# Optimization experiments

Hardware: AMD Instinct MI355X
Metric: run time of the kernel (lower is better)

## Reference

```python
import jax, jax.numpy as jnp
import numpy as np

B, L, D, H = 2, 2048, 1024, 16
HD = D // H  # head_dim = 64


def setup_inputs() -> dict:
    key = jax.random.key(0)
    k1, k2, k3 = jax.random.split(key, 3)
    x = jax.random.normal(k1, (B, L, D), dtype=jnp.float32)
    # nn.Linear(d_model, 3*d_model): weight [3D, D], bias [3D]
    lim = 1.0 / np.sqrt(D)
    W_qkv = jax.random.uniform(k2, (3 * D, D), dtype=jnp.float32, minval=-lim, maxval=lim)
    b_qkv = jax.random.uniform(k3, (3 * D,), dtype=jnp.float32, minval=-lim, maxval=lim)
    return {"x": x, "W_qkv": W_qkv, "b_qkv": b_qkv}


def reference(x, W_qkv, b_qkv):
    b, l, d = x.shape
    qkv = x @ W_qkv.T + b_qkv                      # [b, l, 3d]
    q, k, v = jnp.split(qkv, 3, axis=-1)           # each [b, l, d]
    # split heads: [b, l, h, hd]
    q = q.reshape(b, l, H, HD)
    k = k.reshape(b, l, H, HD)
    v = v.reshape(b, l, H, HD)
    scale = 1.0 / np.sqrt(HD).astype(np.float32)
    # scores [b, h, l, l]
    scores = jnp.einsum('bqhd,bkhd->bhqk', q, k) * scale
    attn = jax.nn.softmax(scores, axis=-1)
    out = jnp.einsum('bhqk,bkhd->bqhd', attn, v)   # [b, l, h, hd]
    return out.reshape(b, l, d)
```

## Files before the change

### kernel.cpp

```cpp
#include <hip/hip_runtime.h>

#define BATCH 2
#define SEQ 2048
#define DMODEL 1024
#define NH 16
#define HD 64
#define M_TOT (BATCH*SEQ)
#define N_TOT (3*DMODEL)
#define K_TOT (DMODEL)

typedef __attribute__((ext_vector_type(8)))  _Float16 f16x8;
typedef __attribute__((ext_vector_type(4)))  float    f32x4;
typedef __attribute__((ext_vector_type(16))) float    f32x16;

static __device__ __forceinline__ unsigned short f2h(float f) {
  _Float16 h = (_Float16)f;
  return __builtin_bit_cast(unsigned short, h);
}

static __device__ __forceinline__ f32x16 zero16() {
  f32x16 z;
  #pragma unroll
  for (int i = 0; i < 16; ++i) z[i] = 0.f;
  return z;
}

static __device__ __forceinline__ void async16(const unsigned short* g, unsigned short* l) {
  __builtin_amdgcn_global_load_lds(
      (const __attribute__((address_space(1))) unsigned*)g,
      (__attribute__((address_space(3))) unsigned*)l, 16, 0, 0);
}

__global__ __launch_bounds__(256) void cast_f16(
    const float* __restrict__ src, unsigned short* __restrict__ dst, int n8)
{
  int i = blockIdx.x * 256 + threadIdx.x;
  if (i >= n8) return;
  float4 v0 = ((const float4*)src)[2*i];
  float4 v1 = ((const float4*)src)[2*i + 1];
  uint4 pk;
  pk.x = (unsigned)f2h(v0.x) | ((unsigned)f2h(v0.y) << 16);
  pk.y = (unsigned)f2h(v0.z) | ((unsigned)f2h(v0.w) << 16);
  pk.z = (unsigned)f2h(v1.x) | ((unsigned)f2h(v1.y) << 16);
  pk.w = (unsigned)f2h(v1.z) | ((unsigned)f2h(v1.w) << 16);
  ((uint4*)dst)[i] = pk;
}

__global__ __launch_bounds__(256) void qkv_gemm_mfma(
    const unsigned short* __restrict__ A,
    const unsigned short* __restrict__ B,
    const float* __restrict__ bias,
    unsigned short* __restrict__ C)
{
  __shared__ unsigned short As[128][32];
  __shared__ unsigned short Bs[128][32];

  const int tid  = threadIdx.x;
  const int wave = tid >> 6;
  const int lane = tid & 63;
  const int l15  = lane & 15;
  const int quad = lane >> 4;

  const int n0 = blockIdx.x * 128;
  const int m0 = blockIdx.y * 128;
  const int wm = (wave & 1) * 64;
  const int wn = (wave >> 1) * 64;

  f32x4 acc[4][4];
  #pragma unroll
  for (int i = 0; i < 4; ++i)
    #pragma unroll
    for (int j = 0; j < 4; ++j) acc[i][j] = (f32x4){0.f,0.f,0.f,0.f};

  const int srow = tid >> 2;
  const int skc  = (tid & 3) * 8;
  const unsigned short* Ag0 = A + (size_t)(m0 + srow) * K_TOT + skc;
  const unsigned short* Ag1 = A + (size_t)(m0 + 64 + srow) * K_TOT + skc;
  const unsigned short* Bg0 = B + (size_t)(n0 + srow) * K_TOT + skc;
  const unsigned short* Bg1 = B + (size_t)(n0 + 64 + srow) * K_TOT + skc;
  unsigned short* Al0 = &As[0][0] + tid * 8;
  unsigned short* Al1 = Al0 + 2048;
  unsigned short* Bl0 = &Bs[0][0] + tid * 8;
  unsigned short* Bl1 = Bl0 + 2048;

  for (int k0 = 0; k0 < K_TOT; k0 += 32) {
    __syncthreads();
    async16(Ag0 + k0, Al0);
    async16(Ag1 + k0, Al1);
    async16(Bg0 + k0, Bl0);
    async16(Bg1 + k0, Bl1);
    __syncthreads();

    f16x8 af[4], bf[4];
    #pragma unroll
    for (int i = 0; i < 4; ++i)
      af[i] = *(const f16x8*)&As[wm + i*16 + l15][quad*8];
    #pragma unroll
    for (int j = 0; j < 4; ++j)
      bf[j] = *(const f16x8*)&Bs[wn + j*16 + l15][quad*8];

    #pragma unroll
    for (int i = 0; i < 4; ++i)
      #pragma unroll
      for (int j = 0; j < 4; ++j)
        acc[i][j] = __builtin_amdgcn_mfma_f32_16x16x32_f16(af[i], bf[j], acc[i][j], 0, 0, 0);
  }

  float bv[4];
  #pragma unroll
  for (int j = 0; j < 4; ++j) bv[j] = bias[n0 + wn + j*16 + l15];

  #pragma unroll
  for (int i = 0; i < 4; ++i) {
    #pragma unroll
    for (int j = 0; j < 4; ++j) {
      #pragma unroll
      for (int r = 0; r < 4; ++r) {
        const size_t row = (size_t)(m0 + wm + i*16 + quad*4 + r);
        C[row * N_TOT + n0 + wn + j*16 + l15] = f2h(acc[i][j][r] + bv[j]);
      }
    }
  }
}

__global__ __launch_bounds__(256) void attn_mfma2(
    const unsigned short* __restrict__ qkv, float* __restrict__ out)
{
  __shared__ unsigned short Ks[64][72];
  __shared__ unsigned short Vt[64][72];
  __shared__ unsigned short Ps[4][32][72];
  __shared__ float Dn[4][32];

  const int tid  = threadIdx.x;
  const int wv   = tid >> 6;
  const int lane = tid & 63;
  const int l31  = lane & 31;
  const int h32  = lane >> 5;
  const int qsw  = l31 >> 3;

  const int qt = blockIdx.x;
  const int hh = blockIdx.y;
  const int b  = blockIdx.z;
  const int q0 = qt*128 + wv*32;

  f16x8 qf[4];
  {
    const unsigned short* qrow = qkv + (size_t)(b*SEQ + q0 + l31) * N_TOT + hh*HD;
    #pragma unroll
    for (int f = 0; f < 4; ++f)
      qf[f] = *(const f16x8*)(qrow + f*16 + h32*8);
  }

  f32x16 oacc[2];
  oacc[0] = zero16();
  oacc[1] = zero16();
  float dsum = 0.f;

  const unsigned short* kg = qkv + (size_t)b*SEQ*N_TOT + DMODEL   + hh*HD;
  const unsigned short* vg = qkv + (size_t)b*SEQ*N_TOT + 2*DMODEL + hh*HD;

  for (int kt = 0; kt < SEQ/64; ++kt) {
    const int k0 = kt * 64;
    __syncthreads();

    #pragma unroll
    for (int i = 0; i < 2; ++i) {
      int f   = tid + 256*i;
      int key = f >> 3, c = f & 7;
      const unsigned short* src = kg + (size_t)(k0 + key) * N_TOT + c*8;
      int sc = c ^ ((key >> 3) & 7);
      *(uint4*)&Ks[key][sc*8] = *(const uint4*)src;
    }
    {
      int key = tid >> 2;
      int d0  = (tid & 3) * 16;
      const unsigned short* src = vg + (size_t)(k0 + key) * N_TOT + d0;
      union { uint4 v; unsigned short s[8]; } u0, u1;
      u0.v = *(const uint4*)src;
      u1.v = *(const uint4*)(src + 8);
      const int kgrp = key >> 3, klow = key & 7;
      #pragma unroll
      for (int j = 0; j < 8; ++j) {
        int dd = d0 + j;
        Vt[dd][((kgrp ^ ((dd >> 3) & 7)) * 8) + klow] = u0.s[j];
        dd = d0 + 8 + j;
        Vt[dd][((kgrp ^ ((dd >> 3) & 7)) * 8) + klow] = u1.s[j];
      }
    }
    __syncthreads();

    f32x16 sa[2];
    sa[0] = zero16();
    sa[1] = zero16();
    #pragma unroll
    for (int f = 0; f < 4; ++f) {
      const int g = f*2 + h32;
      #pragma unroll
      for (int kb = 0; kb < 2; ++kb) {
        const int row = kb*32 + l31;
        f16x8 kf = *(const f16x8*)&Ks[row][((g ^ ((row >> 3) & 7)) * 8)];
        sa[kb] = __builtin_amdgcn_mfma_f32_32x32x16_f16(kf, qf[f], sa[kb], 0, 0, 0);
      }
    }

    #pragma unroll
    for (int kb = 0; kb < 2; ++kb) {
      #pragma unroll
      for (int g4 = 0; g4 < 4; ++g4) {
        unsigned short hsv[4];
        #pragma unroll
        for (int r = 0; r < 4; ++r) {
          float p = __expf(0.125f * sa[kb][g4*4 + r]);
          dsum += p;
          hsv[r] = f2h(p);
        }
        unsigned short* dst =
            &Ps[wv][l31][(((kb*4 + g4) ^ qsw) & 7) * 8 + h32*4];
        uint2 pk;
        pk.x = (unsigned)hsv[0] | ((unsigned)hsv[1] << 16);
        pk.y = (unsigned)hsv[2] | ((unsigned)hsv[3] << 16);
        *(uint2*)dst = pk;
      }
    }

    #pragma unroll
    for (int f = 0; f < 4; ++f) {
      const int g = f*2 + h32;
      f16x8 pf = *(const f16x8*)&Ps[wv][l31][((g ^ qsw) & 7) * 8];
      #pragma unroll
      for (int jd = 0; jd < 2; ++jd) {
        const int row = jd*32 + l31;
        f16x8 vf = *(const f16x8*)&Vt[row][((g ^ ((row >> 3) & 7)) * 8)];
        oacc[jd] = __builtin_amdgcn_mfma_f32_32x32x16_f16(pf, vf, oacc[jd], 0, 0, 0);
      }
    }
  }

  dsum += __shfl_xor(dsum, 32, 64);
  Dn[wv][l31] = 1.f / dsum;

  #pragma unroll
  for (int jd = 0; jd < 2; ++jd) {
    #pragma unroll
    for (int g4 = 0; g4 < 4; ++g4) {
      #pragma unroll
      for (int r = 0; r < 4; ++r) {
        const int qrow = g4*8 + h32*4 + r;
        const float oval = oacc[jd][g4*4 + r] * Dn[wv][qrow];
        out[(size_t)(b*SEQ + q0 + qrow) * DMODEL + hh*HD + jd*32 + l31] = oval;
      }
    }
  }
}

extern "C" void kernel_launch(void* const* d_in, const int* in_sizes, int n_in,
                              void* d_out, int out_size, void* d_ws, size_t ws_size,
                              hipStream_t stream) {
  const float* x    = (const float*)d_in[0];
  const float* W    = (const float*)d_in[1];
  const float* bias = (const float*)d_in[2];
  float* out = (float*)d_out;

  unsigned short* qkv = (unsigned short*)d_ws;
  unsigned short* xh  = qkv + (size_t)M_TOT * N_TOT;
  unsigned short* Wh  = xh  + (size_t)M_TOT * K_TOT;

  cast_f16<<<(M_TOT*K_TOT/8 + 255)/256, 256, 0, stream>>>(x, xh, M_TOT*K_TOT/8);
  cast_f16<<<(N_TOT*K_TOT/8 + 255)/256, 256, 0, stream>>>(W, Wh, N_TOT*K_TOT/8);

  dim3 g1(N_TOT/128, M_TOT/128);
  qkv_gemm_mfma<<<g1, 256, 0, stream>>>(xh, Wh, bias, qkv);

  dim3 g2(SEQ/128, NH, BATCH);
  attn_mfma2<<<g2, 256, 0, stream>>>(qkv, out);
}
```

Baseline: 191.4 us.

## Emit transposed V from GEMM, double-buffer async K/V loads in attention

The QKV GEMM now writes Q and K into a packed buffer, with Q pre-scaled by log2(e)/sqrt(hd), and computes V^T directly by swapping operands so V lands per head in transposed layout. The GEMM K-step grows to 64 with a rotated LDS swizzle. The attention kernel uses global_load_lds to double-buffer K and V tiles, with manual waitcnt and barriers. It also switches to exp2f and raises wave priority around the MFMA blocks. This removes the per-tile scalar transposition of V in LDS and overlaps loads with compute, at the cost of more LDS and scattered V^T stores in the GEMM epilogue.

```diff
diff --git a/kernel.cpp b/kernel.cpp
--- a/kernel.cpp
+++ b/kernel.cpp
@@ -8,6 +8,8 @@
 #define M_TOT (BATCH*SEQ)
 #define N_TOT (3*DMODEL)
 #define K_TOT (DMODEL)
+#define NQK   (2*DMODEL)
+#define QSCALE 0.18033688011112042f
 
 typedef __attribute__((ext_vector_type(8)))  _Float16 f16x8;
 typedef __attribute__((ext_vector_type(4)))  float    f32x4;
@@ -47,13 +49,14 @@
 }
 
 __global__ __launch_bounds__(256) void qkv_gemm_mfma(
-    const unsigned short* __restrict__ A,
-    const unsigned short* __restrict__ B,
+    const unsigned short* __restrict__ Xh,
+    const unsigned short* __restrict__ Wh,
     const float* __restrict__ bias,
-    unsigned short* __restrict__ C)
+    unsigned short* __restrict__ QK,
+    unsigned short* __restrict__ VT)
 {
-  __shared__ unsigned short As[128][32];
-  __shared__ unsigned short Bs[128][32];
+  __shared__ unsigned short As[128][64];
+  __shared__ unsigned short Bs[128][64];
 
   const int tid  = threadIdx.x;
   const int wave = tid >> 6;
@@ -61,8 +64,19 @@
   const int l15  = lane & 15;
   const int quad = lane >> 4;
 
-  const int n0 = blockIdx.x * 128;
+  const bool isV = (blockIdx.x >= (NQK/128));
+  const int n0 = (isV ? (blockIdx.x - NQK/128) : blockIdx.x) * 128;
   const int m0 = blockIdx.y * 128;
+
+  const unsigned short* Arows = isV ? (Wh + (size_t)(NQK + n0) * K_TOT)
+                                    : (Xh + (size_t)m0 * K_TOT);
+  const unsigned short* Brows = isV ? (Xh + (size_t)m0 * K_TOT)
+                                    : (Wh + (size_t)n0 * K_TOT);
+
+  const int sr = tid >> 3;
+  const int sp = tid & 7;
+  const int sg = ((sp - sr) & 7) * 8;
+
   const int wm = (wave & 1) * 64;
   const int wn = (wave >> 1) * 64;
 
@@ -72,62 +86,75 @@
     #pragma unroll
     for (int j = 0; j < 4; ++j) acc[i][j] = (f32x4){0.f,0.f,0.f,0.f};
 
-  const int srow = tid >> 2;
-  const int skc  = (tid & 3) * 8;
-  const unsigned short* Ag0 = A + (size_t)(m0 + srow) * K_TOT + skc;
-  const unsigned short* Ag1 = A + (size_t)(m0 + 64 + srow) * K_TOT + skc;
-  const unsigned short* Bg0 = B + (size_t)(n0 + srow) * K_TOT + skc;
-  const unsigned short* Bg1 = B + (size_t)(n0 + 64 + srow) * K_TOT + skc;
-  unsigned short* Al0 = &As[0][0] + tid * 8;
-  unsigned short* Al1 = Al0 + 2048;
-  unsigned short* Bl0 = &Bs[0][0] + tid * 8;
-  unsigned short* Bl1 = Bl0 + 2048;
-
-  for (int k0 = 0; k0 < K_TOT; k0 += 32) {
+  for (int k0 = 0; k0 < K_TOT; k0 += 64) {
     __syncthreads();
-    async16(Ag0 + k0, Al0);
-    async16(Ag1 + k0, Al1);
-    async16(Bg0 + k0, Bl0);
-    async16(Bg1 + k0, Bl1);
+    #pragma unroll
+    for (int s = 0; s < 4; ++s) {
+      async16(Arows + (size_t)(s*32 + sr) * K_TOT + k0 + sg, &As[0][0] + s*2048 + tid*8);
+      async16(Brows + (size_t)(s*32 + sr) * K_TOT + k0 + sg, &Bs[0][0] + s*2048 + tid*8);
+    }
     __syncthreads();
 
-    f16x8 af[4], bf[4];
+    #pragma unroll
+    for (int h = 0; h < 2; ++h) {
+      f16x8 af[4], bf[4];
+      #pragma unroll
+      for (int i = 0; i < 4; ++i) {
+        const int r = wm + i*16 + l15;
+        af[i] = *(const f16x8*)&As[r][((h*4 + quad + r) & 7) * 8];
+      }
+      #pragma unroll
+      for (int j = 0; j < 4; ++j) {
+        const int r = wn + j*16 + l15;
+        bf[j] = *(const f16x8*)&Bs[r][((h*4 + quad + r) & 7) * 8];
+      }
+      #pragma unroll
+      for (int i = 0; i < 4; ++i)
+        #pragma unroll
+        for (int j = 0; j < 4; ++j)
+          acc[i][j] = __builtin_amdgcn_mfma_f32_16x16x32_f16(af[i], bf[j], acc[i][j], 0, 0, 0);
+    }
+  }
+
+  if (!isV) {
+    const float sc = (n0 < DMODEL) ? QSCALE : 1.0f;
+    float bv[4];
+    #pragma unroll
+    for (int j = 0; j < 4; ++j) bv[j] = bias[n0 + wn + j*16 + l15];
     #pragma unroll
     for (int i = 0; i < 4; ++i)
-      af[i] = *(const f16x8*)&As[wm + i*16 + l15][quad*8];
-    #pragma unroll
-    for (int j = 0; j < 4; ++j)
-      bf[j] = *(const f16x8*)&Bs[wn + j*16 + l15][quad*8];
-
+      #pragma unroll
+      for (int j = 0; j < 4; ++j)
+        #pragma unroll
+        for (int r = 0; r < 4; ++r) {
+          const size_t row = (size_t)(m0 + wm + i*16 + quad*4 + r);
+          QK[row * NQK + n0 + wn + j*16 + l15] = f2h((acc[i][j][r] + bv[j]) * sc);
+        }
+  } else {
+    const int bidx  = m0 >> 11;
+    const int sbase = (m0 & 2047) + wn;
     #pragma unroll
     for (int i = 0; i < 4; ++i)
       #pragma unroll
-      for (int j = 0; j < 4; ++j)
-        acc[i][j] = __builtin_amdgcn_mfma_f32_16x16x32_f16(af[i], bf[j], acc[i][j], 0, 0, 0);
-  }
-
-  float bv[4];
-  #pragma unroll
-  for (int j = 0; j < 4; ++j) bv[j] = bias[n0 + wn + j*16 + l15];
-
-  #pragma unroll
-  for (int i = 0; i < 4; ++i) {
-    #pragma unroll
-    for (int j = 0; j < 4; ++j) {
-      #pragma unroll
       for (int r = 0; r < 4; ++r) {
-        const size_t row = (size_t)(m0 + wm + i*16 + quad*4 + r);
-        C[row * N_TOT + n0 + wn + j*16 + l15] = f2h(acc[i][j][r] + bv[j]);
-      }
-    }
-  }
-}
-
-__global__ __launch_bounds__(256) void attn_mfma2(
-    const unsigned short* __restrict__ qkv, float* __restrict__ out)
+        const int nn = n0 + wm + i*16 + quad*4 + r;
+        const float bb = bias[NQK + nn];
+        unsigned short* drow =
+            VT + ((size_t)(bidx*NH + (nn >> 6)) * HD + (nn & 63)) * SEQ + sbase;
+        #pragma unroll
+        for (int j = 0; j < 4; ++j)
+          drow[j*16 + l15] = f2h(acc[i][j][r] + bb);
+      }
+  }
+}
+
+__global__ __launch_bounds__(256) void attn_mfma3(
+    const unsigned short* __restrict__ QK,
+    const unsigned short* __restrict__ VT,
+    float* __restrict__ out)
 {
-  __shared__ unsigned short Ks[64][72];
-  __shared__ unsigned short Vt[64][72];
+  __shared__ unsigned short Ks[2][64][64];
+  __shared__ unsigned short Vs[2][64][64];
   __shared__ unsigned short Ps[4][32][72];
   __shared__ float Dn[4][32];
 
@@ -145,63 +172,59 @@
 
   f16x8 qf[4];
   {
-    const unsigned short* qrow = qkv + (size_t)(b*SEQ + q0 + l31) * N_TOT + hh*HD;
+    const unsigned short* qrow = QK + (size_t)(b*SEQ + q0 + l31) * NQK + hh*HD;
     #pragma unroll
     for (int f = 0; f < 4; ++f)
       qf[f] = *(const f16x8*)(qrow + f*16 + h32*8);
   }
+
+  const unsigned short* Kg = QK + (size_t)b*SEQ*NQK + DMODEL + hh*HD;
+  const unsigned short* Vg = VT + (size_t)(b*NH + hh) * HD * SEQ;
+
+  const int sr = tid >> 3;
+  const int sp = tid & 7;
+  const int sg = ((sp - sr) & 7) * 8;
+
+  const unsigned short* kg0 = Kg + (size_t)sr      * NQK + sg;
+  const unsigned short* kg1 = Kg + (size_t)(sr+32) * NQK + sg;
+  const unsigned short* vg0 = Vg + (size_t)sr      * SEQ + sg;
+  const unsigned short* vg1 = Vg + (size_t)(sr+32) * SEQ + sg;
+  unsigned short* kl = &Ks[0][0][0] + tid*8;
+  unsigned short* vl = &Vs[0][0][0] + tid*8;
 
   f32x16 oacc[2];
   oacc[0] = zero16();
   oacc[1] = zero16();
   float dsum = 0.f;
 
-  const unsigned short* kg = qkv + (size_t)b*SEQ*N_TOT + DMODEL   + hh*HD;
-  const unsigned short* vg = qkv + (size_t)b*SEQ*N_TOT + 2*DMODEL + hh*HD;
-
-  for (int kt = 0; kt < SEQ/64; ++kt) {
-    const int k0 = kt * 64;
-    __syncthreads();
-
-    #pragma unroll
-    for (int i = 0; i < 2; ++i) {
-      int f   = tid + 256*i;
-      int key = f >> 3, c = f & 7;
-      const unsigned short* src = kg + (size_t)(k0 + key) * N_TOT + c*8;
-      int sc = c ^ ((key >> 3) & 7);
-      *(uint4*)&Ks[key][sc*8] = *(const uint4*)src;
-    }
-    {
-      int key = tid >> 2;
-      int d0  = (tid & 3) * 16;
-      const unsigned short* src = vg + (size_t)(k0 + key) * N_TOT + d0;
-      union { uint4 v; unsigned short s[8]; } u0, u1;
-      u0.v = *(const uint4*)src;
-      u1.v = *(const uint4*)(src + 8);
-      const int kgrp = key >> 3, klow = key & 7;
-      #pragma unroll
-      for (int j = 0; j < 8; ++j) {
-        int dd = d0 + j;
-        Vt[dd][((kgrp ^ ((dd >> 3) & 7)) * 8) + klow] = u0.s[j];
-        dd = d0 + 8 + j;
-        Vt[dd][((kgrp ^ ((dd >> 3) & 7)) * 8) + klow] = u1.s[j];
-      }
-    }
-    __syncthreads();
+  auto STAGE = [&](int kt, int bb) {
+    const size_t krow = (size_t)kt * 64 * NQK;
+    const int    kcol = kt * 64;
+    async16(kg0 + krow, kl + bb*4096);
+    async16(kg1 + krow, kl + bb*4096 + 2048);
+    async16(vg0 + kcol, vl + bb*4096);
+    async16(vg1 + kcol, vl + bb*4096 + 2048);
+  };
+
+  auto COMPUTE = [&](int bb) {
+    const unsigned short* ks = &Ks[bb][0][0];
+    const unsigned short* vs = &Vs[bb][0][0];
 
     f32x16 sa[2];
     sa[0] = zero16();
     sa[1] = zero16();
+    __builtin_amdgcn_s_setprio(1);
     #pragma unroll
     for (int f = 0; f < 4; ++f) {
       const int g = f*2 + h32;
       #pragma unroll
       for (int kb = 0; kb < 2; ++kb) {
         const int row = kb*32 + l31;
-        f16x8 kf = *(const f16x8*)&Ks[row][((g ^ ((row >> 3) & 7)) * 8)];
+        f16x8 kf = *(const f16x8*)(ks + row*64 + ((g + row) & 7) * 8);
         sa[kb] = __builtin_amdgcn_mfma_f32_32x32x16_f16(kf, qf[f], sa[kb], 0, 0, 0);
       }
     }
+    __builtin_amdgcn_s_setprio(0);
 
     #pragma unroll
     for (int kb = 0; kb < 2; ++kb) {
@@ -210,7 +233,7 @@
         unsigned short hsv[4];
         #pragma unroll
         for (int r = 0; r < 4; ++r) {
-          float p = __expf(0.125f * sa[kb][g4*4 + r]);
+          float p = exp2f(sa[kb][g4*4 + r]);
           dsum += p;
           hsv[r] = f2h(p);
         }
@@ -223,6 +246,7 @@
       }
     }
 
+    __builtin_amdgcn_s_setprio(1);
     #pragma unroll
     for (int f = 0; f < 4; ++f) {
       const int g = f*2 + h32;
@@ -230,11 +254,25 @@
       #pragma unroll
       for (int jd = 0; jd < 2; ++jd) {
         const int row = jd*32 + l31;
-        f16x8 vf = *(const f16x8*)&Vt[row][((g ^ ((row >> 3) & 7)) * 8)];
+        f16x8 vf = *(const f16x8*)(vs + row*64 + ((g + row) & 7) * 8);
         oacc[jd] = __builtin_amdgcn_mfma_f32_32x32x16_f16(pf, vf, oacc[jd], 0, 0, 0);
       }
     }
-  }
+    __builtin_amdgcn_s_setprio(0);
+  };
+
+  STAGE(0, 0);
+  for (int kt = 0; kt < SEQ/64 - 1; ++kt) {
+    STAGE(kt + 1, (kt + 1) & 1);
+    asm volatile("s_waitcnt vmcnt(4)" ::: "memory");
+    __builtin_amdgcn_s_barrier();
+    COMPUTE(kt & 1);
+    asm volatile("" ::: "memory");
+    __builtin_amdgcn_s_barrier();
+  }
+  asm volatile("s_waitcnt vmcnt(0)" ::: "memory");
+  __builtin_amdgcn_s_barrier();
+  COMPUTE((SEQ/64 - 1) & 1);
 
   dsum += __shfl_xor(dsum, 32, 64);
   Dn[wv][l31] = 1.f / dsum;
@@ -261,16 +299,17 @@
   const float* bias = (const float*)d_in[2];
   float* out = (float*)d_out;
 
-  unsigned short* qkv = (unsigned short*)d_ws;
-  unsigned short* xh  = qkv + (size_t)M_TOT * N_TOT;
-  unsigned short* Wh  = xh  + (size_t)M_TOT * K_TOT;
+  unsigned short* qk = (unsigned short*)d_ws;
+  unsigned short* vt = qk + (size_t)M_TOT * NQK;
+  unsigned short* xh = vt + (size_t)BATCH * NH * HD * SEQ;
+  unsigned short* wh = xh + (size_t)M_TOT * K_TOT;
 
   cast_f16<<<(M_TOT*K_TOT/8 + 255)/256, 256, 0, stream>>>(x, xh, M_TOT*K_TOT/8);
-  cast_f16<<<(N_TOT*K_TOT/8 + 255)/256, 256, 0, stream>>>(W, Wh, N_TOT*K_TOT/8);
+  cast_f16<<<(N_TOT*K_TOT/8 + 255)/256, 256, 0, stream>>>(W, wh, N_TOT*K_TOT/8);
 
   dim3 g1(N_TOT/128, M_TOT/128);
-  qkv_gemm_mfma<<<g1, 256, 0, stream>>>(xh, Wh, bias, qkv);
+  qkv_gemm_mfma<<<g1, 256, 0, stream>>>(xh, wh, bias, qk, vt);
 
   dim3 g2(SEQ/128, NH, BATCH);
-  attn_mfma2<<<g2, 256, 0, stream>>>(qkv, out);
-}
+  attn_mfma3<<<g2, 256, 0, stream>>>(qk, vt, out);
+}
```

After: 186.3 us. -2.7%, faster.
